# Kernel tuning notes

Hardware: AMD Instinct MI355X
Metric: run time of the kernel (lower is better)

## Reference

```python
import math
import jax, jax.numpy as jnp
import numpy as np

B, L, D = 8, 4096, 1024
H = 8
DK = D // H          # d_keys = d_values = 128
K_FACTOR = 2


def setup_inputs() -> dict:
    key = jax.random.key(0)
    ks = jax.random.split(key, 11)
    s = 0.02
    return {
        "queries": jax.random.normal(ks[0], (B, L, D), dtype=jnp.float32),
        "keys":    jax.random.normal(ks[1], (B, L, D), dtype=jnp.float32),
        "values":  jax.random.normal(ks[2], (B, L, D), dtype=jnp.float32),
        "Wq": jax.random.normal(ks[3], (D, H * DK), dtype=jnp.float32) * s,
        "bq": jnp.zeros((H * DK,), dtype=jnp.float32),
        "Wk": jax.random.normal(ks[4], (D, H * DK), dtype=jnp.float32) * s,
        "bk": jnp.zeros((H * DK,), dtype=jnp.float32),
        "Wv": jax.random.normal(ks[5], (D, H * DK), dtype=jnp.float32) * s,
        "bv": jnp.zeros((H * DK,), dtype=jnp.float32),
        "Wo": jax.random.normal(ks[6], (H * DK, D), dtype=jnp.float32) * s,
        "bo": jnp.zeros((D,), dtype=jnp.float32),
    }


def reference(queries, keys, values, Wq, bq, Wk, bk, Wv, bv, Wo, bo):
    b, l, _ = queries.shape
    # projections + head split: [B, L, H, DK]
    q = (queries @ Wq + bq).reshape(b, l, H, DK)
    k = (keys @ Wk + bk).reshape(b, l, H, DK)
    v = (values @ Wv + bv).reshape(b, l, H, DK)
    # L == S so the pad/truncate branch is a no-op (keys[:, :L] == keys)

    qT = q.transpose(0, 2, 3, 1)  # [B, H, DK, L]
    kT = k.transpose(0, 2, 3, 1)
    vT = v.transpose(0, 2, 3, 1)

    # FFT-based circular cross-correlation along time axis
    q_fft = jnp.fft.rfft(qT, axis=-1)
    k_fft = jnp.fft.rfft(kT, axis=-1)
    corr = jnp.fft.irfft(q_fft * jnp.conj(k_fft), n=l, axis=-1)  # [B, H, DK, L]

    # time-delay aggregation over top-k delays
    top_k = int(K_FACTOR * math.log(l))
    weights, delay = jax.lax.top_k(corr, top_k)        # [B, H, DK, K]
    tmp_corr = jax.nn.softmax(weights, axis=-1)
    tmp_values = jnp.concatenate([vT, vT], axis=-1)    # [B, H, DK, 2L] circular wrap
    init_index = jnp.arange(l)

    delay_k = jnp.moveaxis(delay, -1, 0)               # [K, B, H, DK]
    corr_k = jnp.moveaxis(tmp_corr, -1, 0)             # [K, B, H, DK]

    def step(acc, dc):
        d_i, c_i = dc                                  # [B, H, DK]
        idx = init_index[None, None, None, :] + d_i[..., None]   # [B, H, DK, L]
        pattern = jnp.take_along_axis(tmp_values, idx, axis=-1)
        return acc + pattern * c_i[..., None], None

    agg, _ = jax.lax.scan(step, jnp.zeros_like(vT), (delay_k, corr_k))

    out = agg.transpose(0, 3, 1, 2).reshape(b, l, H * DK)  # [B, L, H*DK]
    return out @ Wo + bo
```

## Files before the change

### kernel.cpp

```cpp
#include <hip/hip_runtime.h>
#include <hip/hip_bf16.h>
#include <string.h>

#define NB 8
#define LSEQ 4096
#define DMOD 1024
#define NCH (NB * DMOD)
#define TOPK 16

typedef unsigned short u16;
typedef unsigned int u32;
typedef __attribute__((ext_vector_type(4))) float f32x4;
typedef __attribute__((ext_vector_type(8))) _Float16 f16x8;

__device__ __forceinline__ float h2f(u16 u) {
  _Float16 h;
  __builtin_memcpy(&h, &u, 2);
  return (float)h;
}
__device__ __forceinline__ u16 f2h(float f) {
  _Float16 h = (_Float16)f;
  u16 u;
  __builtin_memcpy(&u, &h, 2);
  return u;
}
__device__ __forceinline__ u32 pk2(float a, float b) {
  return (u32)f2h(a) | ((u32)f2h(b) << 16);
}
__device__ __forceinline__ float2 cmul(float2 a, float2 b) {
  return make_float2(a.x * b.x - a.y * b.y, a.x * b.y + a.y * b.x);
}
__device__ __forceinline__ float2 cmul_conj(float2 a, float2 b) {
  return make_float2(a.x * b.x + a.y * b.y, a.y * b.x - a.x * b.y);
}

__global__ __launch_bounds__(256) void twiddle_k(float2* tw) {
  int i = blockIdx.x * 256 + threadIdx.x;
  if (i < 4096) {
    float ang = -2.0f * 3.14159265358979323846f * (float)i / 4096.0f;
    tw[i] = make_float2(cosf(ang), sinf(ang));
  }
}

__global__ __launch_bounds__(256) void transpose_w_k(const float* __restrict__ src,
                                                     u16* __restrict__ dst,
                                                     int R, int C) {
  __shared__ u16 tile[64][66];
  int c0 = blockIdx.x * 64, r0 = blockIdx.y * 64;
  int tx = threadIdx.x & 63, ty = threadIdx.x >> 6;
#pragma unroll
  for (int i = 0; i < 16; i++) {
    int r = ty + i * 4;
    tile[r][tx] = f2h(src[(size_t)(r0 + r) * C + c0 + tx]);
  }
  __syncthreads();
#pragma unroll
  for (int i = 0; i < 16; i++) {
    int cc = ty + i * 4;
    dst[(size_t)(c0 + cc) * R + r0 + tx] = tile[tx][cc];
  }
}

__global__ __launch_bounds__(256) void gemm_proj_k(const float* __restrict__ A,
                                                   const u16* __restrict__ Btw,
                                                   const float* __restrict__ bias,
                                                   u16* __restrict__ out,
                                                   int K) {
  __shared__ __align__(16) u16 smem[17408];
  u16* As = smem;
  u16* Bs = smem + 5120;
  int tid = threadIdx.x;
  int lane = tid & 63, wave = tid >> 6;
  int quad = lane >> 4, l15 = lane & 15;
  int m0 = blockIdx.y * 128, n0 = blockIdx.x * 128;
  int wm = (wave >> 1) * 64, wn = (wave & 1) * 64;
  int r_a = tid >> 2, kc = (tid & 3) * 8;

  f32x4 acc[4][4];
#pragma unroll
  for (int i = 0; i < 4; i++)
#pragma unroll
    for (int j = 0; j < 4; j++)
      acc[i][j] = (f32x4){0.f, 0.f, 0.f, 0.f};

  for (int kk = 0; kk < K; kk += 32) {
    __syncthreads();
    const float* ga0 = A + (size_t)(m0 + r_a) * K + kk + kc;
    const float* ga1 = ga0 + (size_t)64 * K;
    float4 x0 = *(const float4*)ga0;
    float4 x1 = *(const float4*)(ga0 + 4);
    float4 y0 = *(const float4*)ga1;
    float4 y1 = *(const float4*)(ga1 + 4);
    uint4 wa, wb;
    wa.x = pk2(x0.x, x0.y); wa.y = pk2(x0.z, x0.w);
    wa.z = pk2(x1.x, x1.y); wa.w = pk2(x1.z, x1.w);
    wb.x = pk2(y0.x, y0.y); wb.y = pk2(y0.z, y0.w);
    wb.z = pk2(y1.x, y1.y); wb.w = pk2(y1.z, y1.w);
    *(uint4*)&As[r_a * 40 + kc] = wa;
    *(uint4*)&As[(r_a + 64) * 40 + kc] = wb;
    const u16* gb = Btw + (size_t)(n0 + r_a) * K + kk + kc;
    *(uint4*)&Bs[r_a * 40 + kc] = *(const uint4*)gb;
    *(uint4*)&Bs[(r_a + 64) * 40 + kc] = *(const uint4*)(gb + (size_t)64 * K);
    __syncthreads();
    f16x8 af[4], bfr[4];
    int ka = quad * 8;
#pragma unroll
    for (int i = 0; i < 4; i++)
      af[i] = *(const f16x8*)&As[(wm + i * 16 + l15) * 40 + ka];
#pragma unroll
    for (int j = 0; j < 4; j++)
      bfr[j] = *(const f16x8*)&Bs[(wn + j * 16 + l15) * 40 + ka];
#pragma unroll
    for (int i = 0; i < 4; i++)
#pragma unroll
      for (int j = 0; j < 4; j++)
        acc[i][j] = __builtin_amdgcn_mfma_f32_16x16x32_f16(af[i], bfr[j], acc[i][j], 0, 0, 0);
  }

  __syncthreads();
  float bv[4];
#pragma unroll
  for (int j = 0; j < 4; j++) bv[j] = bias[n0 + wn + j * 16 + l15];
  u16* Ct = smem;
#pragma unroll
  for (int i = 0; i < 4; i++) {
#pragma unroll
    for (int j = 0; j < 4; j++) {
      int ml = wm + i * 16 + quad * 4;
      int nl = wn + j * 16 + l15;
      unsigned long long pkv = 0;
#pragma unroll
      for (int r = 0; r < 4; r++)
        pkv |= ((unsigned long long)f2h(acc[i][j][r] + bv[j])) << (16 * r);
      *(unsigned long long*)&Ct[nl * 136 + ml] = pkv;
    }
  }
  __syncthreads();
  int b_ = m0 >> 12, t0 = m0 & 4095;
#pragma unroll
  for (int it = 0; it < 8; it++) {
    int row = (tid >> 4) + it * 16;
    int col = (tid & 15) * 8;
    uint4 v = *(const uint4*)&Ct[row * 136 + col];
    *(uint4*)(out + (size_t)b_ * DMOD * LSEQ + (size_t)(n0 + row) * LSEQ + t0 + col) = v;
  }
}

__global__ __launch_bounds__(256) void gemm_tA_k(const u16* __restrict__ Acm,
                                                 const u16* __restrict__ Wot,
                                                 const float* __restrict__ bias,
                                                 float* __restrict__ out) {
  __shared__ __align__(16) u16 smem[17408];
  u32* Ta = (u32*)smem;
  u16* Bs = smem + 4224;
  int tid = threadIdx.x;
  int lane = tid & 63, wave = tid >> 6;
  int quad = lane >> 4, l15 = lane & 15;
  int b = blockIdx.z;
  int m0 = blockIdx.y * 128, n0 = blockIdx.x * 128;
  int wm = (wave >> 1) * 64, wn = (wave & 1) * 64;
  int cp = tid >> 4, t0s = (tid & 15) * 8;
  int r_b = tid >> 2, kc = (tid & 3) * 8;
  const u16* Ab = Acm + (size_t)b * DMOD * LSEQ;

  f32x4 acc[4][4];
#pragma unroll
  for (int i = 0; i < 4; i++)
#pragma unroll
    for (int j = 0; j < 4; j++)
      acc[i][j] = (f32x4){0.f, 0.f, 0.f, 0.f};

  for (int kk = 0; kk < DMOD; kk += 32) {
    __syncthreads();
    const u16* ga = Ab + (size_t)(kk + 2 * cp) * LSEQ + m0 + t0s;
    uint4 v0 = *(const uint4*)ga;
    uint4 v1 = *(const uint4*)(ga + LSEQ);
    int tb = cp * 132 + t0s;
    uint4 w0, w1;
    w0.x = (v0.x & 0xffffu) | (v1.x << 16);
    w0.y = (v0.x >> 16) | (v1.x & 0xffff0000u);
    w0.z = (v0.y & 0xffffu) | (v1.y << 16);
    w0.w = (v0.y >> 16) | (v1.y & 0xffff0000u);
    w1.x = (v0.z & 0xffffu) | (v1.z << 16);
    w1.y = (v0.z >> 16) | (v1.z & 0xffff0000u);
    w1.z = (v0.w & 0xffffu) | (v1.w << 16);
    w1.w = (v0.w >> 16) | (v1.w & 0xffff0000u);
    *(uint4*)&Ta[tb] = w0;
    *(uint4*)&Ta[tb + 4] = w1;
    const u16* gb = Wot + (size_t)(n0 + r_b) * DMOD + kk + kc;
    *(uint4*)&Bs[r_b * 40 + kc] = *(const uint4*)gb;
    *(uint4*)&Bs[(r_b + 64) * 40 + kc] = *(const uint4*)(gb + (size_t)64 * DMOD);
    __syncthreads();
    f16x8 af[4], bfr[4];
    int ka = quad * 8;
#pragma unroll
    for (int i = 0; i < 4; i++) {
      int mrow = wm + i * 16 + l15;
      uint4 fa;
      fa.x = Ta[(quad * 4 + 0) * 132 + mrow];
      fa.y = Ta[(quad * 4 + 1) * 132 + mrow];
      fa.z = Ta[(quad * 4 + 2) * 132 + mrow];
      fa.w = Ta[(quad * 4 + 3) * 132 + mrow];
      af[i] = *(f16x8*)&fa;
    }
#pragma unroll
    for (int j = 0; j < 4; j++)
      bfr[j] = *(const f16x8*)&Bs[(wn + j * 16 + l15) * 40 + ka];
#pragma unroll
    for (int i = 0; i < 4; i++)
#pragma unroll
      for (int j = 0; j < 4; j++)
        acc[i][j] = __builtin_amdgcn_mfma_f32_16x16x32_f16(af[i], bfr[j], acc[i][j], 0, 0, 0);
  }

  float bv[4];
#pragma unroll
  for (int j = 0; j < 4; j++) bv[j] = bias[n0 + wn + j * 16 + l15];
  float* Cf = (float*)smem;
#pragma unroll
  for (int half = 0; half < 2; half++) {
    __syncthreads();
    if ((wave >> 1) == half) {
#pragma unroll
      for (int i = 0; i < 4; i++) {
#pragma unroll
        for (int j = 0; j < 4; j++) {
          int mlocal = i * 16 + quad * 4;
          int nl = wn + j * 16 + l15;
#pragma unroll
          for (int r = 0; r < 4; r++)
            Cf[(mlocal + r) * 132 + nl] = acc[i][j][r] + bv[j];
        }
      }
    }
    __syncthreads();
#pragma unroll
    for (int it = 0; it < 8; it++) {
      int row = (tid >> 5) + it * 8;
      int col = (tid & 31) * 4;
      float4 v = *(const float4*)&Cf[row * 132 + col];
      *(float4*)(out + (size_t)b * LSEQ * DMOD +
                 (size_t)(m0 + half * 64 + row) * DMOD + n0 + col) = v;
    }
  }
}

#define SWZ(t) ((t) ^ (((t) >> 4) & 15))

#define FOREACH16(M) M(0) M(1) M(2) M(3) M(4) M(5) M(6) M(7) \
                     M(8) M(9) M(10) M(11) M(12) M(13) M(14) M(15)
#define BITREV16(M) M(0,0) M(1,8) M(2,4) M(3,12) M(4,2) M(5,10) M(6,6) M(7,14) \
                    M(8,1) M(9,9) M(10,5) M(11,13) M(12,3) M(13,11) M(14,7) M(15,15)

#define BF(a, b) { float tx = (b).x, ty = (b).y; \
                   (b).x = (a).x - tx; (b).y = (a).y - ty; \
                   (a).x += tx; (a).y += ty; }
#define BFW(a, b, wr, wi) { float tx = (b).x*(wr) - (b).y*(wi); \
                            float ty = (b).x*(wi) + (b).y*(wr); \
                            (b).x = (a).x - tx; (b).y = (a).y - ty; \
                            (a).x += tx; (a).y += ty; }

#define FFT_SQ 0.70710678118654752440f
#define FFT_C1 0.92387953251128675613f
#define FFT_S1 0.38268343236508977173f

#define DFT16(SGc) \
  BF(z0,z1) BF(z2,z3) BF(z4,z5) BF(z6,z7) BF(z8,z9) BF(z10,z11) BF(z12,z13) BF(z14,z15) \
  BF(z0,z2) BFW(z1,z3,0.f,(SGc)) BF(z4,z6) BFW(z5,z7,0.f,(SGc)) \
  BF(z8,z10) BFW(z9,z11,0.f,(SGc)) BF(z12,z14) BFW(z13,z15,0.f,(SGc)) \
  BF(z0,z4) BFW(z1,z5,FFT_SQ,(SGc)*FFT_SQ) BFW(z2,z6,0.f,(SGc)) BFW(z3,z7,-FFT_SQ,(SGc)*FFT_SQ) \
  BF(z8,z12) BFW(z9,z13,FFT_SQ,(SGc)*FFT_SQ) BFW(z10,z14,0.f,(SGc)) BFW(z11,z15,-FFT_SQ,(SGc)*FFT_SQ) \
  BF(z0,z8) BFW(z1,z9,FFT_C1,(SGc)*FFT_S1) BFW(z2,z10,FFT_SQ,(SGc)*FFT_SQ) BFW(z3,z11,FFT_S1,(SGc)*FFT_C1) \
  BFW(z4,z12,0.f,(SGc)) BFW(z5,z13,-FFT_S1,(SGc)*FFT_C1) BFW(z6,z14,-FFT_SQ,(SGc)*FFT_SQ) BFW(z7,z15,-FFT_C1,(SGc)*FFT_S1)

__global__ __launch_bounds__(256, 4)
void fft_corr_topk_k(const u16* __restrict__ Qt,
                     const u16* __restrict__ Kt,
                     const float2* __restrict__ tw,
                     float* __restrict__ topw,
                     int* __restrict__ topd) {
  __shared__ float2 buf[4096];
  __shared__ float candv[256];
  __shared__ int candi[256];
  __shared__ float tvs[TOPK];
  __shared__ int tds[TOPK];
  __shared__ int winner;
  int ch = blockIdx.x;
  int tid = threadIdx.x;
  const u16* qrow = Qt + (size_t)ch * LSEQ;
  const u16* krow = Kt + (size_t)ch * LSEQ;
  const int jj = tid >> 4, k16 = tid & 15;

#define DECLZ(u) float2 z##u;
  FOREACH16(DECLZ)

#define LD1(r, k) { int t = tid + 256 * (r); \
                    z##k = make_float2(h2f(qrow[t]), h2f(krow[t])); }
  BITREV16(LD1)
  DFT16(-1.f)
#define ST1(u) { float2 w = tw[((u) * tid) & 4095]; \
                 buf[SWZ(16 * tid + (u))] = cmul(z##u, w); }
  FOREACH16(ST1)
  __syncthreads();

#define LD2(r, k) z##k = buf[SWZ(tid + 256 * (r))];
  BITREV16(LD2)
  __syncthreads();
  DFT16(-1.f)
#define ST2F(u) { float2 w = tw[((u) * jj * 16) & 4095]; \
                  buf[SWZ(256 * jj + k16 + 16 * (u))] = cmul(z##u, w); }
  FOREACH16(ST2F)
  __syncthreads();

  BITREV16(LD2)
  __syncthreads();
  DFT16(-1.f)
#define ST3(u) buf[SWZ(tid + 256 * (u))] = z##u;
  FOREACH16(ST3)
  __syncthreads();

#define LDP(r, k) { int t = tid + 256 * (r); \
                    float2 zf = buf[SWZ(t)]; \
                    float2 zn = buf[SWZ((4096 - t) & 4095)]; \
                    float ax = zf.x + zn.x, ay = zf.y - zn.y; \
                    float dx = zf.x - zn.x, dy = zf.y + zn.y; \
                    float px = ax * dx + ay * dy; \
                    float py = ay * dx - ax * dy; \
                    z##k = make_float2(-0.25f * py, 0.25f * px); }
  BITREV16(LDP)
  __syncthreads();
  DFT16(1.f)
#define ST1I(u) { float2 w = tw[((u) * tid) & 4095]; \
                  buf[SWZ(16 * tid + (u))] = cmul_conj(z##u, w); }
  FOREACH16(ST1I)
  __syncthreads();

  BITREV16(LD2)
  __syncthreads();
  DFT16(1.f)
#define ST2I(u) { float2 w = tw[((u) * jj * 16) & 4095]; \
                  buf[SWZ(256 * jj + k16 + 16 * (u))] = cmul_conj(z##u, w); }
  FOREACH16(ST2I)
  __syncthreads();

  BITREV16(LD2)
  DFT16(1.f)
#define DECLV(u) float v##u = z##u.x;
  FOREACH16(DECLV)

  const float NEGINF = -__builtin_inff();
  {
    float bvv = v0;
    int bu = 0;
#define AMX(u) if (v##u > bvv) { bvv = v##u; bu = (u); }
    AMX(1) AMX(2) AMX(3) AMX(4) AMX(5) AMX(6) AMX(7)
    AMX(8) AMX(9) AMX(10) AMX(11) AMX(12) AMX(13) AMX(14) AMX(15)
    candv[tid] = bvv;
    candi[tid] = tid + (bu << 8);
  }
  for (int r = 0; r < TOPK; r++) {
    __syncthreads();
    if (tid < 64) {
      float v0r = candv[tid];
      int i0r = candi[tid];
#pragma unroll
      for (int s2 = 1; s2 < 4; s2++) {
        float v1r = candv[tid + 64 * s2];
        int i1r = candi[tid + 64 * s2];
        if (v1r > v0r || (v1r == v0r && i1r < i0r)) { v0r = v1r; i0r = i1r; }
      }
#pragma unroll
      for (int off = 32; off > 0; off >>= 1) {
        float ov = __shfl_down(v0r, off);
        int oi = __shfl_down(i0r, off);
        if (ov > v0r || (ov == v0r && oi < i0r)) { v0r = ov; i0r = oi; }
      }
      if (tid == 0) { tvs[r] = v0r; tds[r] = i0r; winner = i0r; }
    }
    __syncthreads();
    int wnr = winner;
    if ((wnr & 255) == tid) {
      int ku = wnr >> 8;
#define KILLV(u) if (ku == (u)) v##u = NEGINF;
      FOREACH16(KILLV)
      float bvv = v0;
      int bu = 0;
      AMX(1) AMX(2) AMX(3) AMX(4) AMX(5) AMX(6) AMX(7)
      AMX(8) AMX(9) AMX(10) AMX(11) AMX(12) AMX(13) AMX(14) AMX(15)
      candv[tid] = bvv;
      candi[tid] = tid + (bu << 8);
    }
  }
  __syncthreads();
  if (tid == 0) {
    float mx = tvs[0];
    float e[TOPK];
    float s = 0.f;
#pragma unroll
    for (int k2 = 0; k2 < TOPK; k2++) {
      e[k2] = __expf((tvs[k2] - mx) * (1.0f / 4096.0f));
      s += e[k2];
    }
    float inv = 1.0f / s;
#pragma unroll
    for (int k2 = 0; k2 < TOPK; k2++) {
      topw[(size_t)ch * TOPK + k2] = e[k2] * inv;
      topd[(size_t)ch * TOPK + k2] = tds[k2];
    }
  }
}

__global__ __launch_bounds__(256) void aggregate_k(const u16* __restrict__ Vt,
                                                   const float* __restrict__ topw,
                                                   const int* __restrict__ topd,
                                                   u16* __restrict__ agg) {
  __shared__ u16 vrow[4096];
  __shared__ float w_s[TOPK];
  __shared__ int d_s[TOPK];
  int ch = blockIdx.x, tid = threadIdx.x;
  const u16* src = Vt + (size_t)ch * LSEQ;
#pragma unroll
  for (int p = 0; p < 16; p++) vrow[tid + p * 256] = src[tid + p * 256];
  if (tid < TOPK) {
    w_s[tid] = topw[(size_t)ch * TOPK + tid];
    d_s[tid] = topd[(size_t)ch * TOPK + tid];
  }
  __syncthreads();
#pragma unroll
  for (int p = 0; p < 16; p++) {
    int t = tid + p * 256;
    float s = 0.f;
#pragma unroll
    for (int k = 0; k < TOPK; k++)
      s += w_s[k] * h2f(vrow[(t + d_s[k]) & 4095]);
    agg[(size_t)ch * LSEQ + t] = f2h(s);
  }
}

extern "C" void kernel_launch(void* const* d_in, const int* in_sizes, int n_in,
                              void* d_out, int out_size, void* d_ws, size_t ws_size,
                              hipStream_t stream) {
  (void)in_sizes; (void)n_in; (void)out_size; (void)ws_size;
  const float* queries = (const float*)d_in[0];
  const float* keys    = (const float*)d_in[1];
  const float* values  = (const float*)d_in[2];
  const float* Wq = (const float*)d_in[3];
  const float* bq = (const float*)d_in[4];
  const float* Wk = (const float*)d_in[5];
  const float* bk = (const float*)d_in[6];
  const float* Wv = (const float*)d_in[7];
  const float* bv = (const float*)d_in[8];
  const float* Wo = (const float*)d_in[9];
  const float* bo = (const float*)d_in[10];

  char* ws = (char*)d_ws;
  u16* ws0 = (u16*)ws;
  u16* Wqt = (u16*)(ws + (64ull << 20));
  u16* Wkt = Wqt + 1024 * 1024;
  u16* Wvt = Wkt + 1024 * 1024;
  u16* Wot = Wvt + 1024 * 1024;
  float2* tw = (float2*)(ws + (72ull << 20));
  float* topw = (float*)(ws + (72ull << 20) + (64ull << 10));
  int* topd = (int*)(ws + (72ull << 20) + (64ull << 10) + (512ull << 10));

  u16* Qt = ws0;
  u16* Kt = (u16*)d_out;
  u16* Vt = (u16*)d_out;
  u16* agg = ws0;

  twiddle_k<<<dim3(16), dim3(256), 0, stream>>>(tw);
  transpose_w_k<<<dim3(16, 16), dim3(256), 0, stream>>>(Wq, Wqt, 1024, 1024);
  transpose_w_k<<<dim3(16, 16), dim3(256), 0, stream>>>(Wk, Wkt, 1024, 1024);
  transpose_w_k<<<dim3(16, 16), dim3(256), 0, stream>>>(Wv, Wvt, 1024, 1024);
  transpose_w_k<<<dim3(16, 16), dim3(256), 0, stream>>>(Wo, Wot, 1024, 1024);
  dim3 gg(8, 256);
  gemm_proj_k<<<gg, dim3(256), 0, stream>>>(queries, Wqt, bq, Qt, 1024);
  gemm_proj_k<<<gg, dim3(256), 0, stream>>>(keys, Wkt, bk, Kt, 1024);
  fft_corr_topk_k<<<dim3(NCH), dim3(256), 0, stream>>>(Qt, Kt, tw, topw, topd);
  gemm_proj_k<<<gg, dim3(256), 0, stream>>>(values, Wvt, bv, Vt, 1024);
  aggregate_k<<<dim3(NCH), dim3(256), 0, stream>>>(Vt, topw, topd, agg);
  gemm_tA_k<<<dim3(8, 32, 8), dim3(256), 0, stream>>>(agg, Wot, bo, (float*)d_out);
}
```

Before: 1.439 ms.

## Restructure FFT correlation kernel from radix-16 three-pass to radix-8 four-pass with 512 threads

The 4096-point FFT and inverse FFT per channel now use four radix-8 passes with 512 threads, instead of three radix-16 passes with 256 threads. Each thread holds 8 complex values instead of 16, which lowers register pressure and doubles threads per block. The aim is better latency hiding. The cost is one extra shared-memory pass with its barriers in each direction, plus a wider candidate reduction in the top-k stage.

```diff
diff --git a/kernel.cpp b/kernel.cpp
--- a/kernel.cpp
+++ b/kernel.cpp
@@ -247,10 +247,8 @@
 
 #define SWZ(t) ((t) ^ (((t) >> 4) & 15))
 
-#define FOREACH16(M) M(0) M(1) M(2) M(3) M(4) M(5) M(6) M(7) \
-                     M(8) M(9) M(10) M(11) M(12) M(13) M(14) M(15)
-#define BITREV16(M) M(0,0) M(1,8) M(2,4) M(3,12) M(4,2) M(5,10) M(6,6) M(7,14) \
-                    M(8,1) M(9,9) M(10,5) M(11,13) M(12,3) M(13,11) M(14,7) M(15,15)
+#define FOREACH8(M) M(0) M(1) M(2) M(3) M(4) M(5) M(6) M(7)
+#define BITREV8(M) M(0,0) M(1,4) M(2,2) M(3,6) M(4,1) M(5,5) M(6,3) M(7,7)
 
 #define BF(a, b) { float tx = (b).x, ty = (b).y; \
                    (b).x = (a).x - tx; (b).y = (a).y - ty; \
@@ -261,27 +259,21 @@
                             (a).x += tx; (a).y += ty; }
 
 #define FFT_SQ 0.70710678118654752440f
-#define FFT_C1 0.92387953251128675613f
-#define FFT_S1 0.38268343236508977173f
-
-#define DFT16(SGc) \
-  BF(z0,z1) BF(z2,z3) BF(z4,z5) BF(z6,z7) BF(z8,z9) BF(z10,z11) BF(z12,z13) BF(z14,z15) \
+
+#define DFT8(SGc) \
+  BF(z0,z1) BF(z2,z3) BF(z4,z5) BF(z6,z7) \
   BF(z0,z2) BFW(z1,z3,0.f,(SGc)) BF(z4,z6) BFW(z5,z7,0.f,(SGc)) \
-  BF(z8,z10) BFW(z9,z11,0.f,(SGc)) BF(z12,z14) BFW(z13,z15,0.f,(SGc)) \
-  BF(z0,z4) BFW(z1,z5,FFT_SQ,(SGc)*FFT_SQ) BFW(z2,z6,0.f,(SGc)) BFW(z3,z7,-FFT_SQ,(SGc)*FFT_SQ) \
-  BF(z8,z12) BFW(z9,z13,FFT_SQ,(SGc)*FFT_SQ) BFW(z10,z14,0.f,(SGc)) BFW(z11,z15,-FFT_SQ,(SGc)*FFT_SQ) \
-  BF(z0,z8) BFW(z1,z9,FFT_C1,(SGc)*FFT_S1) BFW(z2,z10,FFT_SQ,(SGc)*FFT_SQ) BFW(z3,z11,FFT_S1,(SGc)*FFT_C1) \
-  BFW(z4,z12,0.f,(SGc)) BFW(z5,z13,-FFT_S1,(SGc)*FFT_C1) BFW(z6,z14,-FFT_SQ,(SGc)*FFT_SQ) BFW(z7,z15,-FFT_C1,(SGc)*FFT_S1)
-
-__global__ __launch_bounds__(256, 4)
+  BF(z0,z4) BFW(z1,z5,FFT_SQ,(SGc)*FFT_SQ) BFW(z2,z6,0.f,(SGc)) BFW(z3,z7,-FFT_SQ,(SGc)*FFT_SQ)
+
+__global__ __launch_bounds__(512)
 void fft_corr_topk_k(const u16* __restrict__ Qt,
                      const u16* __restrict__ Kt,
                      const float2* __restrict__ tw,
                      float* __restrict__ topw,
                      int* __restrict__ topd) {
   __shared__ float2 buf[4096];
-  __shared__ float candv[256];
-  __shared__ int candi[256];
+  __shared__ float candv[512];
+  __shared__ int candi[512];
   __shared__ float tvs[TOPK];
   __shared__ int tds[TOPK];
   __shared__ int winner;
@@ -289,37 +281,46 @@
   int tid = threadIdx.x;
   const u16* qrow = Qt + (size_t)ch * LSEQ;
   const u16* krow = Kt + (size_t)ch * LSEQ;
-  const int jj = tid >> 4, k16 = tid & 15;
+  const int j1 = tid >> 3, k1 = tid & 7;
+  const int j2 = tid >> 6, k2_ = tid & 63;
 
 #define DECLZ(u) float2 z##u;
-  FOREACH16(DECLZ)
-
-#define LD1(r, k) { int t = tid + 256 * (r); \
+  FOREACH8(DECLZ)
+
+#define LDG(r, k) { int t = tid + 512 * (r); \
                     z##k = make_float2(h2f(qrow[t]), h2f(krow[t])); }
-  BITREV16(LD1)
-  DFT16(-1.f)
-#define ST1(u) { float2 w = tw[((u) * tid) & 4095]; \
-                 buf[SWZ(16 * tid + (u))] = cmul(z##u, w); }
-  FOREACH16(ST1)
-  __syncthreads();
-
-#define LD2(r, k) z##k = buf[SWZ(tid + 256 * (r))];
-  BITREV16(LD2)
-  __syncthreads();
-  DFT16(-1.f)
-#define ST2F(u) { float2 w = tw[((u) * jj * 16) & 4095]; \
-                  buf[SWZ(256 * jj + k16 + 16 * (u))] = cmul(z##u, w); }
-  FOREACH16(ST2F)
-  __syncthreads();
-
-  BITREV16(LD2)
-  __syncthreads();
-  DFT16(-1.f)
-#define ST3(u) buf[SWZ(tid + 256 * (u))] = z##u;
-  FOREACH16(ST3)
-  __syncthreads();
-
-#define LDP(r, k) { int t = tid + 256 * (r); \
+  BITREV8(LDG)
+  DFT8(-1.f)
+#define ST0F(u) { float2 w = tw[((u) * tid) & 4095]; \
+                  buf[SWZ(8 * tid + (u))] = cmul(z##u, w); }
+  FOREACH8(ST0F)
+  __syncthreads();
+
+#define LDS8(r, k) z##k = buf[SWZ(tid + 512 * (r))];
+  BITREV8(LDS8)
+  __syncthreads();
+  DFT8(-1.f)
+#define ST1F(u) { float2 w = tw[((u) * j1 * 8) & 4095]; \
+                  buf[SWZ(64 * j1 + k1 + 8 * (u))] = cmul(z##u, w); }
+  FOREACH8(ST1F)
+  __syncthreads();
+
+  BITREV8(LDS8)
+  __syncthreads();
+  DFT8(-1.f)
+#define ST2F(u) { float2 w = tw[((u) * j2 * 64) & 4095]; \
+                  buf[SWZ(512 * j2 + k2_ + 64 * (u))] = cmul(z##u, w); }
+  FOREACH8(ST2F)
+  __syncthreads();
+
+  BITREV8(LDS8)
+  __syncthreads();
+  DFT8(-1.f)
+#define ST3(u) buf[SWZ(tid + 512 * (u))] = z##u;
+  FOREACH8(ST3)
+  __syncthreads();
+
+#define LDP(r, k) { int t = tid + 512 * (r); \
                     float2 zf = buf[SWZ(t)]; \
                     float2 zn = buf[SWZ((4096 - t) & 4095)]; \
                     float ax = zf.x + zn.x, ay = zf.y - zn.y; \
@@ -327,26 +328,34 @@
                     float px = ax * dx + ay * dy; \
                     float py = ay * dx - ax * dy; \
                     z##k = make_float2(-0.25f * py, 0.25f * px); }
-  BITREV16(LDP)
-  __syncthreads();
-  DFT16(1.f)
-#define ST1I(u) { float2 w = tw[((u) * tid) & 4095]; \
-                  buf[SWZ(16 * tid + (u))] = cmul_conj(z##u, w); }
-  FOREACH16(ST1I)
-  __syncthreads();
-
-  BITREV16(LD2)
-  __syncthreads();
-  DFT16(1.f)
-#define ST2I(u) { float2 w = tw[((u) * jj * 16) & 4095]; \
-                  buf[SWZ(256 * jj + k16 + 16 * (u))] = cmul_conj(z##u, w); }
-  FOREACH16(ST2I)
-  __syncthreads();
-
-  BITREV16(LD2)
-  DFT16(1.f)
+  BITREV8(LDP)
+  __syncthreads();
+  DFT8(1.f)
+#define ST0I(u) { float2 w = tw[((u) * tid) & 4095]; \
+                  buf[SWZ(8 * tid + (u))] = cmul_conj(z##u, w); }
+  FOREACH8(ST0I)
+  __syncthreads();
+
+  BITREV8(LDS8)
+  __syncthreads();
+  DFT8(1.f)
+#define ST1I(u) { float2 w = tw[((u) * j1 * 8) & 4095]; \
+                  buf[SWZ(64 * j1 + k1 + 8 * (u))] = cmul_conj(z##u, w); }
+  FOREACH8(ST1I)
+  __syncthreads();
+
+  BITREV8(LDS8)
+  __syncthreads();
+  DFT8(1.f)
+#define ST2I(u) { float2 w = tw[((u) * j2 * 64) & 4095]; \
+                  buf[SWZ(512 * j2 + k2_ + 64 * (u))] = cmul_conj(z##u, w); }
+  FOREACH8(ST2I)
+  __syncthreads();
+
+  BITREV8(LDS8)
+  DFT8(1.f)
 #define DECLV(u) float v##u = z##u.x;
-  FOREACH16(DECLV)
+  FOREACH8(DECLV)
 
   const float NEGINF = -__builtin_inff();
   {
@@ -354,9 +363,8 @@
     int bu = 0;
 #define AMX(u) if (v##u > bvv) { bvv = v##u; bu = (u); }
     AMX(1) AMX(2) AMX(3) AMX(4) AMX(5) AMX(6) AMX(7)
-    AMX(8) AMX(9) AMX(10) AMX(11) AMX(12) AMX(13) AMX(14) AMX(15)
     candv[tid] = bvv;
-    candi[tid] = tid + (bu << 8);
+    candi[tid] = tid + (bu << 9);
   }
   for (int r = 0; r < TOPK; r++) {
     __syncthreads();
@@ -364,7 +372,7 @@
       float v0r = candv[tid];
       int i0r = candi[tid];
 #pragma unroll
-      for (int s2 = 1; s2 < 4; s2++) {
+      for (int s2 = 1; s2 < 8; s2++) {
         float v1r = candv[tid + 64 * s2];
         int i1r = candi[tid + 64 * s2];
         if (v1r > v0r || (v1r == v0r && i1r < i0r)) { v0r = v1r; i0r = i1r; }
@@ -379,32 +387,28 @@
     }
     __syncthreads();
     int wnr = winner;
-    if ((wnr & 255) == tid) {
-      int ku = wnr >> 8;
+    if ((wnr & 511) == tid) {
+      int ku = wnr >> 9;
 #define KILLV(u) if (ku == (u)) v##u = NEGINF;
-      FOREACH16(KILLV)
+      FOREACH8(KILLV)
       float bvv = v0;
       int bu = 0;
       AMX(1) AMX(2) AMX(3) AMX(4) AMX(5) AMX(6) AMX(7)
-      AMX(8) AMX(9) AMX(10) AMX(11) AMX(12) AMX(13) AMX(14) AMX(15)
       candv[tid] = bvv;
-      candi[tid] = tid + (bu << 8);
+      candi[tid] = tid + (bu << 9);
     }
   }
   __syncthreads();
   if (tid == 0) {
     float mx = tvs[0];
-    float e[TOPK];
     float s = 0.f;
 #pragma unroll
+    for (int k2 = 0; k2 < TOPK; k2++)
+      s += __expf((tvs[k2] - mx) * (1.0f / 4096.0f));
+    float inv = 1.0f / s;
+#pragma unroll
     for (int k2 = 0; k2 < TOPK; k2++) {
-      e[k2] = __expf((tvs[k2] - mx) * (1.0f / 4096.0f));
-      s += e[k2];
-    }
-    float inv = 1.0f / s;
-#pragma unroll
-    for (int k2 = 0; k2 < TOPK; k2++) {
-      topw[(size_t)ch * TOPK + k2] = e[k2] * inv;
+      topw[(size_t)ch * TOPK + k2] = __expf((tvs[k2] - mx) * (1.0f / 4096.0f)) * inv;
       topd[(size_t)ch * TOPK + k2] = tds[k2];
     }
   }
@@ -476,7 +480,7 @@
   dim3 gg(8, 256);
   gemm_proj_k<<<gg, dim3(256), 0, stream>>>(queries, Wqt, bq, Qt, 1024);
   gemm_proj_k<<<gg, dim3(256), 0, stream>>>(keys, Wkt, bk, Kt, 1024);
-  fft_corr_topk_k<<<dim3(NCH), dim3(256), 0, stream>>>(Qt, Kt, tw, topw, topd);
+  fft_corr_topk_k<<<dim3(NCH), dim3(512), 0, stream>>>(Qt, Kt, tw, topw, topd);
   gemm_proj_k<<<gg, dim3(256), 0, stream>>>(values, Wvt, bv, Vt, 1024);
   aggregate_k<<<dim3(NCH), dim3(256), 0, stream>>>(Vt, topw, topd, agg);
   gemm_tA_k<<<dim3(8, 32, 8), dim3(256), 0, stream>>>(agg, Wot, bo, (float*)d_out);
```

Measured after the change: 1.451 ms. About the same (+0.9%).
